# Kernel tuning notes

Measured on AMD Instinct MI355X. Metric: run time of the kernel, lower is better.

The kernel has to match this reference:

```python
import jax, jax.numpy as jnp
import numpy as np

B, I, C, H, W = 8, 16, 256, 64, 64  # batch, instances, channels(=in=out), spatial


def setup_inputs() -> dict:
    key = jax.random.key(0)
    ks = jax.random.split(key, 8)
    x = jax.random.normal(ks[0], (B, C, H, W), dtype=jnp.float32)
    masks = jax.random.uniform(ks[1], (B, I, H, W), dtype=jnp.float32)
    # conv_feat: 1x1 conv C->C  -> weight [C_out, C_in]
    Wf = jax.random.normal(ks[2], (C, C), dtype=jnp.float32) * 0.02
    bf = jax.random.normal(ks[3], (C,), dtype=jnp.float32) * 0.02
    # conv_mask: grouped 1x1 conv, groups=I, each 1 -> C channels -> weight [I, C]
    Wm = jax.random.normal(ks[4], (I, C), dtype=jnp.float32) * 0.02
    bm = jax.random.normal(ks[5], (I, C), dtype=jnp.float32) * 0.02
    # conv_out: 1x1 conv C->C
    Wo = jax.random.normal(ks[6], (C, C), dtype=jnp.float32) * 0.02
    bo = jax.random.normal(ks[7], (C,), dtype=jnp.float32) * 0.02
    gamma = jnp.float32(0.5)  # torch init is 0.0; use nonzero so baseline is nontrivial
    return {"x": x, "masks": masks, "Wf": Wf, "bf": bf, "Wm": Wm, "bm": bm,
            "Wo": Wo, "bo": bo, "gamma": gamma}


def reference(x, masks, Wf, bf, Wm, bm, Wo, bo, gamma):
    b, i, h, w = masks.shape
    c = Wf.shape[0]
    # conv_feat: 1x1 conv == per-pixel matmul
    feat = jnp.einsum('bchw,oc->bohw', x, Wf) + bf[:, None, None]  # [B,C,H,W]
    # grouped 1x1 conv_mask: instance i channel -> C channels
    mc = (masks[:, :, None, :, :] * Wm[None, :, :, None, None]
          + bm[None, :, :, None, None])                              # [B,I,C,H,W]
    # softmax over (C*H*W) per instance, as in masks.view(B, I, -1)
    mc = jax.nn.softmax(mc.reshape(b, i, -1), axis=-1).reshape(b, i, c, h, w)
    # loop sum_i conv_out(feat * mask_i)  ==  conv_out_W @ (feat * sum_i mask_i) + I*bias
    msum = mc.sum(axis=1)                                            # [B,C,H,W]
    out = jnp.einsum('bchw,oc->bohw', feat * msum, Wo) + (i * bo)[:, None, None]
    return gamma * out + x
```

## Files before the change

kernel.cpp:

```cpp
#include <hip/hip_runtime.h>


#define NB 8
#define NI 16
#define NC 256
#define HWSZ 4096
#define PT 64

typedef __attribute__((ext_vector_type(8))) short short8;
typedef __attribute__((ext_vector_type(4))) short short4v;
typedef __attribute__((ext_vector_type(4))) float f32x4;

static __device__ inline short f2bf(float f) {
    unsigned u = __builtin_bit_cast(unsigned, f);
    u += 0x7fffu + ((u >> 16) & 1u);
    return (short)(u >> 16);
}
static __device__ inline float bf2f(short h) {
    unsigned u = ((unsigned)(unsigned short)h) << 16;
    return __builtin_bit_cast(float, u);
}

__global__ __launch_bounds__(256)
void prep_kernel(const float* __restrict__ x, const float* __restrict__ Wf,
                 const float* __restrict__ Wo, short* __restrict__ xTg,
                 short* __restrict__ WfB, short* __restrict__ WoB) {
    const int blk = blockIdx.x, t = threadIdx.x;
    if (blk >= 2048) {
        for (int r = 0; r < 2; ++r) {
            int fid = ((blk - 2048) * 256 + t) * 2 + r;
            const float* src = (fid < 16384) ? Wf : Wo;
            short* dst       = (fid < 16384) ? WfB : WoB;
            int e = (fid & 16383) * 4;
            float4 v = *(const float4*)(src + e);
            short4v o = { f2bf(v.x), f2bf(v.y), f2bf(v.z), f2bf(v.w) };
            *(short4v*)(dst + e) = o;
        }
        return;
    }
    __shared__ float tile[64][65];
    const int b   = blk >> 8;
    const int c0  = ((blk >> 6) & 3) << 6;
    const int hw0 = (blk & 63) << 6;
    const float* xb = x + ((size_t)(b * NC + c0)) * HWSZ + hw0;
#pragma unroll
    for (int it = 0; it < 4; ++it) {
        int idx = it * 256 + t;
        int c = idx >> 4, qq = idx & 15;
        float4 v = *(const float4*)(xb + (size_t)c * HWSZ + qq * 4);
        tile[c][qq * 4 + 0] = v.x; tile[c][qq * 4 + 1] = v.y;
        tile[c][qq * 4 + 2] = v.z; tile[c][qq * 4 + 3] = v.w;
    }
    __syncthreads();
#pragma unroll
    for (int it = 0; it < 2; ++it) {
        int idx = it * 256 + t;
        int hw = idx >> 3, g8 = idx & 7;
        short8 o;
#pragma unroll
        for (int j = 0; j < 8; ++j) o[j] = f2bf(tile[g8 * 8 + j][hw]);
        *(short8*)(xTg + ((size_t)(b * HWSZ + hw0 + hw)) * NC + c0 + g8 * 8) = o;
    }
}

__global__ __launch_bounds__(256)
void stats_kernel(const float* __restrict__ masks, const float* __restrict__ Wm,
                  const float* __restrict__ bm, short* __restrict__ Ahat) {
    const int bi = blockIdx.x;
    const int b  = bi >> 4;
    const int i  = bi & (NI - 1);
    const int t  = threadIdx.x;
    const float* m = masks + (size_t)bi * HWSZ;

    float s1 = 0.f, s2 = 0.f, s3 = 0.f, s4 = 0.f, s5 = 0.f, s6 = 0.f;
    for (int e = t; e < HWSZ; e += 256) {
        float v = m[e];
        float v2 = v * v, v3 = v2 * v;
        s1 += v; s2 += v2; s3 += v3;
        s4 += v2 * v2; s5 += v2 * v3; s6 += v3 * v3;
    }
    __shared__ float red[7][4];
    float sv[6] = { s1, s2, s3, s4, s5, s6 };
#pragma unroll
    for (int k = 0; k < 6; ++k) {
        float v = sv[k];
#pragma unroll
        for (int off = 32; off > 0; off >>= 1) v += __shfl_down(v, off, 64);
        if ((t & 63) == 0) red[k][t >> 6] = v;
    }
    __syncthreads();
    const float S1 = red[0][0] + red[0][1] + red[0][2] + red[0][3];
    const float S2 = red[1][0] + red[1][1] + red[1][2] + red[1][3];
    const float S3 = red[2][0] + red[2][1] + red[2][2] + red[2][3];
    const float S4 = red[3][0] + red[3][1] + red[3][2] + red[3][3];
    const float S5 = red[4][0] + red[4][1] + red[4][2] + red[4][3];
    const float S6 = red[5][0] + red[5][1] + red[5][2] + red[5][3];

    const int c = t;
    const float w  = Wm[i * NC + c];
    const float eb = __expf(bm[i * NC + c]);
    const float poly = (float)HWSZ
        + w * (S1 + w * (0.5f * S2 + w * ((1.f / 6.f) * S3
        + w * ((1.f / 24.f) * S4 + w * ((1.f / 120.f) * S5
        + w * ((1.f / 720.f) * S6))))));
    float v = eb * poly;
#pragma unroll
    for (int off = 32; off > 0; off >>= 1) v += __shfl_down(v, off, 64);
    if ((t & 63) == 0) red[6][t >> 6] = v;
    __syncthreads();
    const float Z = red[6][0] + red[6][1] + red[6][2] + red[6][3];
    const float a = eb / Z;
    short4v av = { f2bf(a), f2bf(a * w), f2bf(a * w * w * 0.5f),
                   f2bf(a * w * w * w * (1.f / 6.f)) };
    *(short4v*)(Ahat + ((size_t)(b * NC + c)) * 64 + i * 4) = av;
}

__global__ __launch_bounds__(256, 2)
void main_kernel(const float* __restrict__ x, const float* __restrict__ masks,
                 const float* __restrict__ bf_, const float* __restrict__ bo,
                 const float* __restrict__ gamma_p, const short* __restrict__ xTg,
                 const short* __restrict__ WfB, const short* __restrict__ WoB,
                 const short* __restrict__ Ahat, float* __restrict__ out) {
    const int blk  = blockIdx.x;
    const int b    = blk >> 6;
    const int hw0  = (blk & 63) << 6;
    const int t    = threadIdx.x;
    const int lane = t & 63;
    const int ln15 = lane & 15;
    const int q    = lane >> 4;
    const int wo0  = (t >> 6) << 6;

    __shared__ short sA[17408];
    __shared__ short sM[4608];
    __shared__ short sZ[16896];

    const short* xsrc = xTg + ((size_t)(b * HWSZ + hw0)) * NC;
#pragma unroll
    for (int it = 0; it < 8; ++it) {
        int idx = it * 256 + t;
        int p = idx >> 5, c8 = idx & 31;
        *(short8*)(sA + p * 264 + c8 * 8) = *(const short8*)(xsrc + p * 256 + c8 * 8);
    }
#pragma unroll
    for (int it = 0; it < 4; ++it) {
        int i = (t >> 6) + it * 4;
        int p = t & 63;
        float m = masks[((size_t)(b * NI + i)) * HWSZ + hw0 + p];
        float m2 = m * m;
        short4v mv = { (short)0x3F80, f2bf(m), f2bf(m2), f2bf(m2 * m) };
        *(short4v*)(sM + p * 72 + i * 4) = mv;
    }
    __syncthreads();

    f32x4 macc[4][4];
#pragma unroll
    for (int ot = 0; ot < 4; ++ot)
#pragma unroll
        for (int pt = 0; pt < 4; ++pt) macc[ot][pt] = (f32x4)0.f;
    const short* Ab = Ahat + ((size_t)b * NC) * 64;
#pragma unroll
    for (int ks = 0; ks < 2; ++ks) {
        short8 af[4], bfr[4];
#pragma unroll
        for (int ot = 0; ot < 4; ++ot)
            af[ot] = *(const short8*)(Ab + (wo0 + ot * 16 + ln15) * 64 + ks * 32 + q * 8);
#pragma unroll
        for (int pt = 0; pt < 4; ++pt)
            bfr[pt] = *(const short8*)(sM + (pt * 16 + ln15) * 72 + ks * 32 + q * 8);
#pragma unroll
        for (int ot = 0; ot < 4; ++ot)
#pragma unroll
            for (int pt = 0; pt < 4; ++pt)
                macc[ot][pt] = __builtin_amdgcn_mfma_f32_16x16x32_bf16(
                    af[ot], bfr[pt], macc[ot][pt], 0, 0, 0);
    }

    f32x4 feat[4][4];
#pragma unroll
    for (int ot = 0; ot < 4; ++ot)
#pragma unroll
        for (int pt = 0; pt < 4; ++pt) feat[ot][pt] = (f32x4)0.f;
#pragma unroll 2
    for (int ks = 0; ks < 8; ++ks) {
        short8 af[4], bfr[4];
#pragma unroll
        for (int ot = 0; ot < 4; ++ot)
            af[ot] = *(const short8*)(WfB + (wo0 + ot * 16 + ln15) * NC + ks * 32 + q * 8);
#pragma unroll
        for (int pt = 0; pt < 4; ++pt)
            bfr[pt] = *(const short8*)(sA + (pt * 16 + ln15) * 264 + ks * 32 + q * 8);
#pragma unroll
        for (int ot = 0; ot < 4; ++ot)
#pragma unroll
            for (int pt = 0; pt < 4; ++pt)
                feat[ot][pt] = __builtin_amdgcn_mfma_f32_16x16x32_bf16(
                    af[ot], bfr[pt], feat[ot][pt], 0, 0, 0);
    }

#pragma unroll
    for (int ot = 0; ot < 4; ++ot) {
        float4 bv = *(const float4*)(bf_ + wo0 + ot * 16 + q * 4);
        float b4[4] = { bv.x, bv.y, bv.z, bv.w };
#pragma unroll
        for (int pt = 0; pt < 4; ++pt) {
            short4v zz;
#pragma unroll
            for (int r = 0; r < 4; ++r)
                zz[r] = f2bf((feat[ot][pt][r] + b4[r]) * macc[ot][pt][r]);
            *(short4v*)(sZ + (pt * 16 + ln15) * 264 + wo0 + ot * 16 + q * 4) = zz;
        }
    }
    __syncthreads();

    f32x4 oacc[4][4];
#pragma unroll
    for (int ot = 0; ot < 4; ++ot)
#pragma unroll
        for (int pt = 0; pt < 4; ++pt) oacc[ot][pt] = (f32x4)0.f;
#pragma unroll 2
    for (int ks = 0; ks < 8; ++ks) {
        short8 af[4], bfr[4];
#pragma unroll
        for (int ot = 0; ot < 4; ++ot)
            af[ot] = *(const short8*)(WoB + (wo0 + ot * 16 + ln15) * NC + ks * 32 + q * 8);
#pragma unroll
        for (int pt = 0; pt < 4; ++pt)
            bfr[pt] = *(const short8*)(sZ + (pt * 16 + ln15) * 264 + ks * 32 + q * 8);
#pragma unroll
        for (int ot = 0; ot < 4; ++ot)
#pragma unroll
            for (int pt = 0; pt < 4; ++pt)
                oacc[ot][pt] = __builtin_amdgcn_mfma_f32_16x16x32_bf16(
                    af[ot], bfr[pt], oacc[ot][pt], 0, 0, 0);
    }

#pragma unroll
    for (int ot = 0; ot < 4; ++ot)
#pragma unroll
        for (int pt = 0; pt < 4; ++pt)
#pragma unroll
            for (int r = 0; r < 4; ++r)
                sA[(wo0 + ot * 16 + q * 4 + r) * 68 + pt * 16 + ln15] =
                    f2bf(oacc[ot][pt][r]);
    __syncthreads();

    const float g = gamma_p[0];
    const float* xb = x + ((size_t)b * NC) * HWSZ + hw0;
    float* ob = out + ((size_t)b * NC) * HWSZ + hw0;
#pragma unroll 4
    for (int it = 0; it < 16; ++it) {
        int idx = it * 256 + t;
        int o = idx >> 4, pq = idx & 15;
        short4v zb = *(const short4v*)(sA + o * 68 + pq * 4);
        float bov = 16.0f * bo[o];
        float4 xv = *(const float4*)(xb + (size_t)o * HWSZ + pq * 4);
        float4 r;
        r.x = g * (bf2f(zb[0]) + bov) + xv.x;
        r.y = g * (bf2f(zb[1]) + bov) + xv.y;
        r.z = g * (bf2f(zb[2]) + bov) + xv.z;
        r.w = g * (bf2f(zb[3]) + bov) + xv.w;
        *(float4*)(ob + (size_t)o * HWSZ + pq * 4) = r;
    }
}

extern "C" void kernel_launch(void* const* d_in, const int* in_sizes, int n_in,
                              void* d_out, int out_size, void* d_ws, size_t ws_size,
                              hipStream_t stream) {
    const float* x     = (const float*)d_in[0];
    const float* masks = (const float*)d_in[1];
    const float* Wf    = (const float*)d_in[2];
    const float* bf    = (const float*)d_in[3];
    const float* Wm    = (const float*)d_in[4];
    const float* bm    = (const float*)d_in[5];
    const float* Wo    = (const float*)d_in[6];
    const float* bo    = (const float*)d_in[7];
    const float* gamma = (const float*)d_in[8];
    float* out = (float*)d_out;

    short* ws   = (short*)d_ws;
    short* xTg  = ws;
    short* WfB  = ws + (size_t)NB * HWSZ * NC;
    short* WoB  = WfB + NC * NC;
    short* Ahat = WoB + NC * NC;

    hipLaunchKernelGGL(prep_kernel, dim3(2048 + 64), dim3(256), 0, stream,
                       x, Wf, Wo, xTg, WfB, WoB);
    hipLaunchKernelGGL(stats_kernel, dim3(NB * NI), dim3(256), 0, stream,
                       masks, Wm, bm, Ahat);
    hipLaunchKernelGGL(main_kernel, dim3(NB * (HWSZ / PT)), dim3(256), 0, stream,
                       x, masks, bf, bo, gamma, xTg, WfB, WoB, Ahat, out);
}
```

Baseline: 132.3 us.

## Fuse x transpose into main kernel and merge prep with stats kernel

Drops the separate pass that transposed x into a bf16 [B,HW,C] global buffer. The main kernel now reads the fp32 x tile directly, transposes it through a double-buffered padded LDS staging area aliased onto sZ, and converts it to bf16 in sA. The weight conversion and mask statistics are merged into one setup kernel, which saves a launch and a round trip of roughly 16MB of intermediate data through global memory. In exchange the main kernel does more LDS work and syncs, and it issues extra loads at the start, which may lengthen its prologue.

```diff
diff --git a/kernel.cpp b/kernel.cpp
--- a/kernel.cpp
+++ b/kernel.cpp
@@ -22,13 +22,16 @@
 }
 
 __global__ __launch_bounds__(256)
-void prep_kernel(const float* __restrict__ x, const float* __restrict__ Wf,
-                 const float* __restrict__ Wo, short* __restrict__ xTg,
-                 short* __restrict__ WfB, short* __restrict__ WoB) {
+void setup_kernel(const float* __restrict__ masks, const float* __restrict__ Wm,
+                  const float* __restrict__ bm, const float* __restrict__ Wf,
+                  const float* __restrict__ Wo, short* __restrict__ Ahat,
+                  short* __restrict__ WfB, short* __restrict__ WoB) {
     const int blk = blockIdx.x, t = threadIdx.x;
-    if (blk >= 2048) {
+    if (blk >= NB * NI) {
+        const int wb = blk - NB * NI;
+#pragma unroll
         for (int r = 0; r < 2; ++r) {
-            int fid = ((blk - 2048) * 256 + t) * 2 + r;
+            int fid = (wb * 256 + t) * 2 + r;
             const float* src = (fid < 16384) ? Wf : Wo;
             short* dst       = (fid < 16384) ? WfB : WoB;
             int e = (fid & 16383) * 4;
@@ -38,38 +41,9 @@
         }
         return;
     }
-    __shared__ float tile[64][65];
-    const int b   = blk >> 8;
-    const int c0  = ((blk >> 6) & 3) << 6;
-    const int hw0 = (blk & 63) << 6;
-    const float* xb = x + ((size_t)(b * NC + c0)) * HWSZ + hw0;
-#pragma unroll
-    for (int it = 0; it < 4; ++it) {
-        int idx = it * 256 + t;
-        int c = idx >> 4, qq = idx & 15;
-        float4 v = *(const float4*)(xb + (size_t)c * HWSZ + qq * 4);
-        tile[c][qq * 4 + 0] = v.x; tile[c][qq * 4 + 1] = v.y;
-        tile[c][qq * 4 + 2] = v.z; tile[c][qq * 4 + 3] = v.w;
-    }
-    __syncthreads();
-#pragma unroll
-    for (int it = 0; it < 2; ++it) {
-        int idx = it * 256 + t;
-        int hw = idx >> 3, g8 = idx & 7;
-        short8 o;
-#pragma unroll
-        for (int j = 0; j < 8; ++j) o[j] = f2bf(tile[g8 * 8 + j][hw]);
-        *(short8*)(xTg + ((size_t)(b * HWSZ + hw0 + hw)) * NC + c0 + g8 * 8) = o;
-    }
-}
-
-__global__ __launch_bounds__(256)
-void stats_kernel(const float* __restrict__ masks, const float* __restrict__ Wm,
-                  const float* __restrict__ bm, short* __restrict__ Ahat) {
-    const int bi = blockIdx.x;
+    const int bi = blk;
     const int b  = bi >> 4;
     const int i  = bi & (NI - 1);
-    const int t  = threadIdx.x;
     const float* m = masks + (size_t)bi * HWSZ;
 
     float s1 = 0.f, s2 = 0.f, s3 = 0.f, s4 = 0.f, s5 = 0.f, s6 = 0.f;
@@ -118,7 +92,7 @@
 __global__ __launch_bounds__(256, 2)
 void main_kernel(const float* __restrict__ x, const float* __restrict__ masks,
                  const float* __restrict__ bf_, const float* __restrict__ bo,
-                 const float* __restrict__ gamma_p, const short* __restrict__ xTg,
+                 const float* __restrict__ gamma_p,
                  const short* __restrict__ WfB, const short* __restrict__ WoB,
                  const short* __restrict__ Ahat, float* __restrict__ out) {
     const int blk  = blockIdx.x;
@@ -130,17 +104,12 @@
     const int q    = lane >> 4;
     const int wo0  = (t >> 6) << 6;
 
-    __shared__ short sA[17408];
-    __shared__ short sM[4608];
-    __shared__ short sZ[16896];
-
-    const short* xsrc = xTg + ((size_t)(b * HWSZ + hw0)) * NC;
-#pragma unroll
-    for (int it = 0; it < 8; ++it) {
-        int idx = it * 256 + t;
-        int p = idx >> 5, c8 = idx & 31;
-        *(short8*)(sA + p * 264 + c8 * 8) = *(const short8*)(xsrc + p * 256 + c8 * 8);
-    }
+    __shared__ __align__(16) short sA[16896];
+    __shared__ __align__(16) short sM[4608];
+    __shared__ __align__(16) short sZ[16896];
+
+    const float* xb = x + ((size_t)b * NC) * HWSZ + hw0;
+
 #pragma unroll
     for (int it = 0; it < 4; ++it) {
         int i = (t >> 6) + it * 4;
@@ -150,6 +119,45 @@
         short4v mv = { (short)0x3F80, f2bf(m), f2bf(m2), f2bf(m2 * m) };
         *(short4v*)(sM + p * 72 + i * 4) = mv;
     }
+
+    float* F = (float*)sZ;
+    float4 xr[4];
+#pragma unroll
+    for (int it = 0; it < 4; ++it) {
+        int idx = it * 256 + t;
+        int c = idx >> 4, qf = idx & 15;
+        xr[it] = *(const float4*)(xb + (size_t)c * HWSZ + qf * 4);
+    }
+    for (int s = 0; s < 4; ++s) {
+        float* Fb = F + (s & 1) * 4160;
+#pragma unroll
+        for (int it = 0; it < 4; ++it) {
+            int idx = it * 256 + t;
+            int c = idx >> 4, qf = idx & 15;
+            Fb[c * 65 + qf * 4 + 0] = xr[it].x;
+            Fb[c * 65 + qf * 4 + 1] = xr[it].y;
+            Fb[c * 65 + qf * 4 + 2] = xr[it].z;
+            Fb[c * 65 + qf * 4 + 3] = xr[it].w;
+        }
+        if (s < 3) {
+#pragma unroll
+            for (int it = 0; it < 4; ++it) {
+                int idx = it * 256 + t;
+                int c = idx >> 4, qf = idx & 15;
+                xr[it] = *(const float4*)(xb + (size_t)((s + 1) * 64 + c) * HWSZ + qf * 4);
+            }
+        }
+        __syncthreads();
+#pragma unroll
+        for (int it2 = 0; it2 < 2; ++it2) {
+            int idx = it2 * 256 + t;
+            int p = idx >> 3, g = idx & 7;
+            short8 o8;
+#pragma unroll
+            for (int j = 0; j < 8; ++j) o8[j] = f2bf(Fb[(g * 8 + j) * 65 + p]);
+            *(short8*)(sA + p * 264 + s * 64 + g * 8) = o8;
+        }
+    }
     __syncthreads();
 
     f32x4 macc[4][4];
@@ -234,6 +242,7 @@
                     af[ot], bfr[pt], oacc[ot][pt], 0, 0, 0);
     }
 
+    __syncthreads();
 #pragma unroll
     for (int ot = 0; ot < 4; ++ot)
 #pragma unroll
@@ -245,7 +254,6 @@
     __syncthreads();
 
     const float g = gamma_p[0];
-    const float* xb = x + ((size_t)b * NC) * HWSZ + hw0;
     float* ob = out + ((size_t)b * NC) * HWSZ + hw0;
 #pragma unroll 4
     for (int it = 0; it < 16; ++it) {
@@ -278,15 +286,12 @@
     float* out = (float*)d_out;
 
     short* ws   = (short*)d_ws;
-    short* xTg  = ws;
-    short* WfB  = ws + (size_t)NB * HWSZ * NC;
+    short* WfB  = ws;
     short* WoB  = WfB + NC * NC;
     short* Ahat = WoB + NC * NC;
 
-    hipLaunchKernelGGL(prep_kernel, dim3(2048 + 64), dim3(256), 0, stream,
-                       x, Wf, Wo, xTg, WfB, WoB);
-    hipLaunchKernelGGL(stats_kernel, dim3(NB * NI), dim3(256), 0, stream,
-                       masks, Wm, bm, Ahat);
+    hipLaunchKernelGGL(setup_kernel, dim3(NB * NI + 64), dim3(256), 0, stream,
+                       masks, Wm, bm, Wf, Wo, Ahat, WfB, WoB);
     hipLaunchKernelGGL(main_kernel, dim3(NB * (HWSZ / PT)), dim3(256), 0, stream,
-                       x, masks, bf, bo, gamma, xTg, WfB, WoB, Ahat, out);
-}
+                       x, masks, bf, bo, gamma, WfB, WoB, Ahat, out);
+}
```

Measured after the change: 126.3 us. -4.5%, faster.
